# Optimization experiments

Measured on AMD Instinct MI355X. Metric: run time of the kernel, lower is better.

The kernel has to match this reference:

```python
import jax, jax.numpy as jnp
import numpy as np

B, TE, TD, H = 8, 512, 256, 256  # batch, enc len, dec len, hidden (He==Hd)

def setup_inputs() -> dict:
    key = jax.random.key(0)
    k1, k2, k3, k4, k5 = jax.random.split(key, 5)
    # Keras 'uniform' initializer: U(-0.05, 0.05)
    u = lambda k, s: jax.random.uniform(k, s, jnp.float32, -0.05, 0.05)
    return {
        "encoder_out_seq": jax.random.normal(k1, (B, TE, H), jnp.float32),
        "decoder_out_seq": jax.random.normal(k2, (B, TD, H), jnp.float32),
        "W_a": u(k3, (H, H)),
        "U_a": u(k4, (H, H)),
        "V_a": u(k5, (H, 1)),
    }

def reference(encoder_out_seq, decoder_out_seq, W_a, U_a, V_a):
    # Bahdanau additive attention, fully batched (same math as the per-step K.rnn loop)
    We = jnp.einsum('bih,hk->bik', encoder_out_seq, W_a)   # [B,Te,H]
    Uh = jnp.einsum('bjh,hk->bjk', decoder_out_seq, U_a)   # [B,Td,H]
    # energies: V_a^T tanh(We_i + Uh_j)  -> [B,Td,Te]
    t = jnp.tanh(We[:, None, :, :] + Uh[:, :, None, :])    # [B,Td,Te,H]
    e = jnp.einsum('bjih,h->bji', t, V_a[:, 0])             # [B,Td,Te]
    e = jax.nn.softmax(e, axis=-1)                          # softmax over encoder positions
    c = jnp.einsum('bji,bih->bjh', e, encoder_out_seq)      # [B,Td,H]
    return (c, e)
```

## Files before the change

kernel.cpp:

```cpp
#include <hip/hip_runtime.h>


#define BB 8
#define TE 512
#define TD 256
#define HH 256

#define EXP2F(x) __builtin_amdgcn_exp2f(x)
#define RCPF(x)  __builtin_amdgcn_rcpf(x)
#define KSCALE   2.8853900817779268f
#define NSC      (-2.8853900817779268f)

typedef __attribute__((ext_vector_type(8))) short short8_t;
typedef __attribute__((ext_vector_type(4))) float f32x4;

__device__ __forceinline__ unsigned short f2bf(float x) {
    unsigned int u = __float_as_uint(x);
    return (unsigned short)((u + 0x7FFFu + ((u >> 16) & 1u)) >> 16);
}
__device__ __forceinline__ float bf2f(unsigned short h) {
    return __uint_as_float(((unsigned int)h) << 16);
}

__global__ __launch_bounds__(256) void k_pre(
    const float* __restrict__ enc, const float* __restrict__ dec,
    const float* __restrict__ Wa,  const float* __restrict__ Ua,
    float* __restrict__ W4, float* __restrict__ Uhe)
{
    const int t  = threadIdx.x;
    const int it = blockIdx.x >> 2;
    const int ht = blockIdx.x & 3;
    const int i0 = it * 64;
    const int h0 = ht * 64;
    const bool is_enc = (i0 < BB * TE);
    const float* X  = is_enc ? (enc + (size_t)i0 * HH)
                             : (dec + (size_t)(i0 - BB * TE) * HH);
    const float* Wg = is_enc ? Wa : Ua;

    __shared__ unsigned short At_h[64][40], At_l[64][40];
    __shared__ unsigned short Xs_h[64][40], Xs_l[64][40];
    __shared__ float T[32][66];

    const int sr = t >> 2;
    const int sq = (t & 3) * 8;
    const int kr = t >> 3;
    const int hc = (t & 7) * 8;

    const int wv = t >> 6, l = t & 63;
    const int wh = (wv & 1) * 32;
    const int wi = (wv >> 1) * 32;
    const int fr = l & 15;
    const int fk = (l >> 4) * 8;
    const int rq = l >> 4;

    f32x4 acc[2][2];
    #pragma unroll
    for (int a0 = 0; a0 < 2; a0++)
        #pragma unroll
        for (int a1 = 0; a1 < 2; a1++)
            acc[a0][a1] = (f32x4){0.f, 0.f, 0.f, 0.f};

    float4 x0  = *(const float4*)(X + (size_t)sr * HH + sq);
    float4 x1  = *(const float4*)(X + (size_t)sr * HH + sq + 4);
    float4 wf0 = *(const float4*)(Wg + (size_t)kr * HH + h0 + hc);
    float4 wf1 = *(const float4*)(Wg + (size_t)kr * HH + h0 + hc + 4);

    #pragma unroll
    for (int c = 0; c < 8; c++) {
        short8_t xh, xl;
        {
            unsigned short h;
            h = f2bf(x0.x); xh[0] = (short)h; xl[0] = (short)f2bf(x0.x - bf2f(h));
            h = f2bf(x0.y); xh[1] = (short)h; xl[1] = (short)f2bf(x0.y - bf2f(h));
            h = f2bf(x0.z); xh[2] = (short)h; xl[2] = (short)f2bf(x0.z - bf2f(h));
            h = f2bf(x0.w); xh[3] = (short)h; xl[3] = (short)f2bf(x0.w - bf2f(h));
            h = f2bf(x1.x); xh[4] = (short)h; xl[4] = (short)f2bf(x1.x - bf2f(h));
            h = f2bf(x1.y); xh[5] = (short)h; xl[5] = (short)f2bf(x1.y - bf2f(h));
            h = f2bf(x1.z); xh[6] = (short)h; xl[6] = (short)f2bf(x1.z - bf2f(h));
            h = f2bf(x1.w); xh[7] = (short)h; xl[7] = (short)f2bf(x1.w - bf2f(h));
        }
        __syncthreads();
        *(short8_t*)&Xs_h[sr][sq] = xh;
        *(short8_t*)&Xs_l[sr][sq] = xl;
        {
            float2 a, b;
            a.x = wf0.x; a.y = wf0.y; b.x = wf0.z; b.y = wf0.w;
            *(float2*)&T[kr][hc]     = a;
            *(float2*)&T[kr][hc + 2] = b;
            a.x = wf1.x; a.y = wf1.y; b.x = wf1.z; b.y = wf1.w;
            *(float2*)&T[kr][hc + 4] = a;
            *(float2*)&T[kr][hc + 6] = b;
        }
        __syncthreads();
        {
            short8_t ah_, al_;
            #pragma unroll
            for (int e = 0; e < 8; e++) {
                float f = T[sq + e][sr];
                unsigned short h = f2bf(f);
                ah_[e] = (short)h;
                al_[e] = (short)f2bf(f - bf2f(h));
            }
            *(short8_t*)&At_h[sr][sq] = ah_;
            *(short8_t*)&At_l[sr][sq] = al_;
        }
        if (c < 7) {
            const int kc = (c + 1) * 32;
            x0  = *(const float4*)(X + (size_t)sr * HH + kc + sq);
            x1  = *(const float4*)(X + (size_t)sr * HH + kc + sq + 4);
            wf0 = *(const float4*)(Wg + (size_t)(kc + kr) * HH + h0 + hc);
            wf1 = *(const float4*)(Wg + (size_t)(kc + kr) * HH + h0 + hc + 4);
        }
        __syncthreads();
        #pragma unroll
        for (int fm = 0; fm < 2; fm++) {
            short8_t a_h = *(const short8_t*)&At_h[wh + 16 * fm + fr][fk];
            short8_t a_l = *(const short8_t*)&At_l[wh + 16 * fm + fr][fk];
            #pragma unroll
            for (int fn = 0; fn < 2; fn++) {
                short8_t b_h = *(const short8_t*)&Xs_h[wi + 16 * fn + fr][fk];
                short8_t b_l = *(const short8_t*)&Xs_l[wi + 16 * fn + fr][fk];
                acc[fm][fn] = __builtin_amdgcn_mfma_f32_16x16x32_bf16(a_h, b_h, acc[fm][fn], 0, 0, 0);
                acc[fm][fn] = __builtin_amdgcn_mfma_f32_16x16x32_bf16(a_h, b_l, acc[fm][fn], 0, 0, 0);
                acc[fm][fn] = __builtin_amdgcn_mfma_f32_16x16x32_bf16(a_l, b_h, acc[fm][fn], 0, 0, 0);
            }
        }
    }

    #pragma unroll
    for (int fm = 0; fm < 2; fm++) {
        #pragma unroll
        for (int fn = 0; fn < 2; fn++) {
            f32x4 v = acc[fm][fn];
            float4 o;
            o.x = EXP2F(v[0] * KSCALE);
            o.y = EXP2F(v[1] * KSCALE);
            o.z = EXP2F(v[2] * KSCALE);
            o.w = EXP2F(v[3] * KSCALE);
            const int ig = i0 + wi + 16 * fn + fr;
            const int hb = h0 + wh + 16 * fm + rq * 4;
            if (is_enc) {
                const int b  = ig >> 9;
                const int ib = ig & 511;
                const int hq = hb >> 2;
                *(float4*)(W4 + (((size_t)b * 64 + hq) * TE + ib) * 4) = o;
            } else {
                const int j = ig - BB * TE;
                *(float4*)(Uhe + (size_t)j * HH + hb) = o;
            }
        }
    }
}

__global__ __launch_bounds__(512) void k_attn(
    const float* __restrict__ enc, const float* __restrict__ W4,
    const float* __restrict__ Uhe, const float* __restrict__ Va,
    float* __restrict__ out_c, float* __restrict__ out_e)
{
    const int wv = threadIdx.x >> 6, lane = threadIdx.x & 63;
    const int b   = blockIdx.x & 7;
    const int j0  = (blockIdx.x >> 3) * 4;
    const int jj0 = b * TD + j0;

    __shared__ float sP[4][TE];
    __shared__ float sR[8][4][HH];

    const int i = (wv << 6) + lane;
    const float* wp = W4 + ((size_t)b * 64 * TE + i) * 4;
    const float* ua = Uhe + (size_t)jj0 * HH;
    const float* va = Va;

    float a0 = 0.f, a1 = 0.f, a2 = 0.f, a3 = 0.f;

#define QSTEP(ACC, U)                                                     \
    {                                                                     \
        float A_ = fmaf(w4.x, (U).x, 1.f);                                \
        float B_ = fmaf(w4.y, (U).y, 1.f);                                \
        float C_ = fmaf(w4.z, (U).z, 1.f);                                \
        float D_ = fmaf(w4.w, (U).w, 1.f);                                \
        float dAB = A_ * B_, dCD = C_ * D_;                               \
        float nAB = fmaf(v4.x, B_, v4.y * A_);                            \
        float nCD = fmaf(v4.z, D_, v4.w * C_);                            \
        float num = fmaf(nAB, dCD, nCD * dAB);                            \
        ACC = fmaf(num, RCPF(dAB * dCD), ACC);                            \
    }

#define ASTEP(Q, W4V)                                                     \
    {                                                                     \
        float4 w4 = W4V;                                                  \
        float4 v4 = *(const float4*)(va + 4 * (Q));                       \
        float4 u0 = *(const float4*)(ua + 4 * (Q));                       \
        float4 u1 = *(const float4*)(ua + HH + 4 * (Q));                  \
        float4 u2 = *(const float4*)(ua + 2 * HH + 4 * (Q));              \
        float4 u3 = *(const float4*)(ua + 3 * HH + 4 * (Q));              \
        QSTEP(a0, u0)                                                     \
        QSTEP(a1, u1)                                                     \
        QSTEP(a2, u2)                                                     \
        QSTEP(a3, u3)                                                     \
    }

    float4 wA = *(const float4*)(wp);
    float4 wB = *(const float4*)(wp + (size_t)TE * 4);
    for (int q = 0; q < 64; q += 2) {
        float4 wC = *(const float4*)(wp + (size_t)(q + 2) * TE * 4);
        float4 wD = *(const float4*)(wp + (size_t)(q + 3) * TE * 4);
        ASTEP(q, wA)
        ASTEP(q + 1, wB)
        wA = wC; wB = wD;
    }
#undef ASTEP
#undef QSTEP

    sP[0][i] = NSC * a0;
    sP[1][i] = NSC * a1;
    sP[2][i] = NSC * a2;
    sP[3][i] = NSC * a3;
    __syncthreads();

    if (wv < 4) {
        float ev[8];
        float m = -3.0e38f;
        #pragma unroll
        for (int k = 0; k < 8; k++) {
            ev[k] = sP[wv][lane + 64 * k];
            m = fmaxf(m, ev[k]);
        }
        #pragma unroll
        for (int off = 32; off; off >>= 1) m = fmaxf(m, __shfl_xor(m, off, 64));
        float s = 0.f;
        #pragma unroll
        for (int k = 0; k < 8; k++) { ev[k] = EXP2F(ev[k] - m); s += ev[k]; }
        #pragma unroll
        for (int off = 32; off; off >>= 1) s += __shfl_xor(s, off, 64);
        float rs = RCPF(s);
        float* oe = out_e + (size_t)(jj0 + wv) * TE;
        #pragma unroll
        for (int k = 0; k < 8; k++) {
            float p = ev[k] * rs;
            sP[wv][lane + 64 * k] = p;
            oe[lane + 64 * k] = p;
        }
    }
    __syncthreads();

    const int ib = wv << 6;
    const float* eb = enc + ((size_t)b * TE + ib) * HH + 4 * lane;
    float4 c0 = {0,0,0,0}, c1 = {0,0,0,0}, c2 = {0,0,0,0}, c3 = {0,0,0,0};

#define BSTEP(K, QV)                                                      \
    {                                                                     \
        float p0 = sP[0][ib + (K)];                                       \
        float p1 = sP[1][ib + (K)];                                       \
        float p2 = sP[2][ib + (K)];                                       \
        float p3 = sP[3][ib + (K)];                                       \
        float4 q = QV;                                                    \
        c0.x = fmaf(p0, q.x, c0.x); c0.y = fmaf(p0, q.y, c0.y);           \
        c0.z = fmaf(p0, q.z, c0.z); c0.w = fmaf(p0, q.w, c0.w);           \
        c1.x = fmaf(p1, q.x, c1.x); c1.y = fmaf(p1, q.y, c1.y);           \
        c1.z = fmaf(p1, q.z, c1.z); c1.w = fmaf(p1, q.w, c1.w);           \
        c2.x = fmaf(p2, q.x, c2.x); c2.y = fmaf(p2, q.y, c2.y);           \
        c2.z = fmaf(p2, q.z, c2.z); c2.w = fmaf(p2, q.w, c2.w);           \
        c3.x = fmaf(p3, q.x, c3.x); c3.y = fmaf(p3, q.y, c3.y);           \
        c3.z = fmaf(p3, q.z, c3.z); c3.w = fmaf(p3, q.w, c3.w);           \
    }

    float4 qA = *(const float4*)(eb);
    float4 qB = *(const float4*)(eb + (size_t)HH);
    for (int k = 0; k < 64; k += 2) {
        const int k2 = (k + 2 < 64) ? k + 2 : 62;
        const int k3 = (k + 3 < 64) ? k + 3 : 63;
        float4 qC = *(const float4*)(eb + (size_t)k2 * HH);
        float4 qD = *(const float4*)(eb + (size_t)k3 * HH);
        BSTEP(k, qA)
        BSTEP(k + 1, qB)
        qA = qC; qB = qD;
    }
#undef BSTEP

    *(float4*)&sR[wv][0][4 * lane] = c0;
    *(float4*)&sR[wv][1][4 * lane] = c1;
    *(float4*)&sR[wv][2][4 * lane] = c2;
    *(float4*)&sR[wv][3][4 * lane] = c3;
    __syncthreads();

    {
        const int jr = wv & 3;
        const int h2 = (wv >> 2) * 128 + 2 * lane;
        float sx = 0.f, sy = 0.f;
        #pragma unroll
        for (int ww = 0; ww < 8; ww++) {
            float2 tv = *(const float2*)&sR[ww][jr][h2];
            sx += tv.x; sy += tv.y;
        }
        float2 o; o.x = sx; o.y = sy;
        *(float2*)(out_c + (size_t)(jj0 + jr) * HH + h2) = o;
    }
}

extern "C" void kernel_launch(void* const* d_in, const int* in_sizes, int n_in,
                              void* d_out, int out_size, void* d_ws, size_t ws_size,
                              hipStream_t stream) {
    const float* enc = (const float*)d_in[0];
    const float* dec = (const float*)d_in[1];
    const float* Wa  = (const float*)d_in[2];
    const float* Ua  = (const float*)d_in[3];
    const float* Va  = (const float*)d_in[4];

    float* W4  = (float*)d_ws;
    float* Uhe = W4 + (size_t)BB * HH * TE;

    float* out_c = (float*)d_out;
    float* out_e = out_c + (size_t)BB * TD * HH;

    k_pre<<<384, 256, 0, stream>>>(enc, dec, Wa, Ua, W4, Uhe);
    k_attn<<<BB * TD / 4, 512, 0, stream>>>(enc, W4, Uhe, Va, out_c, out_e);
}
```

Baseline: 107.8 us.

## Interleave exp tables into 8-wide groups and use packed FP32 math in energy loop

The precompute kernel now writes exp(We) and exp(Uh) in an interleaved 8-float layout that pairs two H-lanes, matching the pairing of the two MFMA fragments. The attention kernel then evaluates the tanh-sum rational form with two-wide float vectors so the compiler can emit packed FMA/mul instructions, halving the scalar VALU op count. V_a is permuted into shared memory to match the new order. This adds a shared-memory staging step and a barrier, and the reciprocals remain scalar.

```diff
diff --git a/kernel.cpp b/kernel.cpp
--- a/kernel.cpp
+++ b/kernel.cpp
@@ -13,6 +13,8 @@
 
 typedef __attribute__((ext_vector_type(8))) short short8_t;
 typedef __attribute__((ext_vector_type(4))) float f32x4;
+typedef __attribute__((ext_vector_type(2))) float f32x2;
+#define PKFMA(a, b, c) __builtin_elementwise_fma((a), (b), (c))
 
 __device__ __forceinline__ unsigned short f2bf(float x) {
     unsigned int u = __float_as_uint(x);
@@ -25,7 +27,7 @@
 __global__ __launch_bounds__(256) void k_pre(
     const float* __restrict__ enc, const float* __restrict__ dec,
     const float* __restrict__ Wa,  const float* __restrict__ Ua,
-    float* __restrict__ W4, float* __restrict__ Uhe)
+    float* __restrict__ W8, float* __restrict__ Uhe2)
 {
     const int t  = threadIdx.x;
     const int it = blockIdx.x >> 2;
@@ -127,34 +129,38 @@
         }
     }
 
+    const int Q0 = (h0 + wh + rq * 4) >> 2;
+    const int p  = ((Q0 >> 3) << 2) | (Q0 & 3);
     #pragma unroll
-    for (int fm = 0; fm < 2; fm++) {
-        #pragma unroll
-        for (int fn = 0; fn < 2; fn++) {
-            f32x4 v = acc[fm][fn];
-            float4 o;
-            o.x = EXP2F(v[0] * KSCALE);
-            o.y = EXP2F(v[1] * KSCALE);
-            o.z = EXP2F(v[2] * KSCALE);
-            o.w = EXP2F(v[3] * KSCALE);
-            const int ig = i0 + wi + 16 * fn + fr;
-            const int hb = h0 + wh + 16 * fm + rq * 4;
-            if (is_enc) {
-                const int b  = ig >> 9;
-                const int ib = ig & 511;
-                const int hq = hb >> 2;
-                *(float4*)(W4 + (((size_t)b * 64 + hq) * TE + ib) * 4) = o;
-            } else {
-                const int j = ig - BB * TE;
-                *(float4*)(Uhe + (size_t)j * HH + hb) = o;
-            }
+    for (int fn = 0; fn < 2; fn++) {
+        f32x4 v0 = acc[0][fn], v1 = acc[1][fn];
+        float4 e0, e1;
+        e0.x = EXP2F(v0[0] * KSCALE); e0.y = EXP2F(v0[1] * KSCALE);
+        e0.z = EXP2F(v0[2] * KSCALE); e0.w = EXP2F(v0[3] * KSCALE);
+        e1.x = EXP2F(v1[0] * KSCALE); e1.y = EXP2F(v1[1] * KSCALE);
+        e1.z = EXP2F(v1[2] * KSCALE); e1.w = EXP2F(v1[3] * KSCALE);
+        float4 lo, hi;
+        lo.x = e0.x; lo.y = e1.x; lo.z = e0.y; lo.w = e1.y;
+        hi.x = e0.z; hi.y = e1.z; hi.z = e0.w; hi.w = e1.w;
+        const int ig = i0 + wi + 16 * fn + fr;
+        if (is_enc) {
+            const int b  = ig >> 9;
+            const int ib = ig & 511;
+            float* dst = W8 + (((size_t)b * 32 + p) * TE + ib) * 8;
+            *(float4*)dst       = lo;
+            *(float4*)(dst + 4) = hi;
+        } else {
+            const int j = ig - BB * TE;
+            float* dst = Uhe2 + (size_t)j * HH + p * 8;
+            *(float4*)dst       = lo;
+            *(float4*)(dst + 4) = hi;
         }
     }
 }
 
 __global__ __launch_bounds__(512) void k_attn(
-    const float* __restrict__ enc, const float* __restrict__ W4,
-    const float* __restrict__ Uhe, const float* __restrict__ Va,
+    const float* __restrict__ enc, const float* __restrict__ W8,
+    const float* __restrict__ Uhe2, const float* __restrict__ Va,
     float* __restrict__ out_c, float* __restrict__ out_e)
 {
     const int wv = threadIdx.x >> 6, lane = threadIdx.x & 63;
@@ -164,57 +170,62 @@
 
     __shared__ float sP[4][TE];
     __shared__ float sR[8][4][HH];
+    __shared__ float sVi[32][8];
+
+    if (threadIdx.x < 256) {
+        const int p = threadIdx.x >> 3, r = threadIdx.x & 7;
+        sVi[p][r] = Va[32 * (p >> 2) + 4 * (p & 3) + 16 * (r & 1) + (r >> 1)];
+    }
+    __syncthreads();
 
     const int i = (wv << 6) + lane;
-    const float* wp = W4 + ((size_t)b * 64 * TE + i) * 4;
-    const float* ua = Uhe + (size_t)jj0 * HH;
-    const float* va = Va;
-
-    float a0 = 0.f, a1 = 0.f, a2 = 0.f, a3 = 0.f;
-
-#define QSTEP(ACC, U)                                                     \
-    {                                                                     \
-        float A_ = fmaf(w4.x, (U).x, 1.f);                                \
-        float B_ = fmaf(w4.y, (U).y, 1.f);                                \
-        float C_ = fmaf(w4.z, (U).z, 1.f);                                \
-        float D_ = fmaf(w4.w, (U).w, 1.f);                                \
-        float dAB = A_ * B_, dCD = C_ * D_;                               \
-        float nAB = fmaf(v4.x, B_, v4.y * A_);                            \
-        float nCD = fmaf(v4.z, D_, v4.w * C_);                            \
-        float num = fmaf(nAB, dCD, nCD * dAB);                            \
-        ACC = fmaf(num, RCPF(dAB * dCD), ACC);                            \
-    }
-
-#define ASTEP(Q, W4V)                                                     \
-    {                                                                     \
-        float4 w4 = W4V;                                                  \
-        float4 v4 = *(const float4*)(va + 4 * (Q));                       \
-        float4 u0 = *(const float4*)(ua + 4 * (Q));                       \
-        float4 u1 = *(const float4*)(ua + HH + 4 * (Q));                  \
-        float4 u2 = *(const float4*)(ua + 2 * HH + 4 * (Q));              \
-        float4 u3 = *(const float4*)(ua + 3 * HH + 4 * (Q));              \
-        QSTEP(a0, u0)                                                     \
-        QSTEP(a1, u1)                                                     \
-        QSTEP(a2, u2)                                                     \
-        QSTEP(a3, u3)                                                     \
-    }
-
-    float4 wA = *(const float4*)(wp);
-    float4 wB = *(const float4*)(wp + (size_t)TE * 4);
-    for (int q = 0; q < 64; q += 2) {
-        float4 wC = *(const float4*)(wp + (size_t)(q + 2) * TE * 4);
-        float4 wD = *(const float4*)(wp + (size_t)(q + 3) * TE * 4);
-        ASTEP(q, wA)
-        ASTEP(q + 1, wB)
-        wA = wC; wB = wD;
-    }
-#undef ASTEP
-#undef QSTEP
-
-    sP[0][i] = NSC * a0;
-    sP[1][i] = NSC * a1;
-    sP[2][i] = NSC * a2;
-    sP[3][i] = NSC * a3;
+    const float* wp = W8 + ((size_t)b * 32 * TE + i) * 8;
+    const float* ua = Uhe2 + (size_t)jj0 * HH;
+
+    f32x2 acc[4];
+    #pragma unroll
+    for (int j = 0; j < 4; j++) acc[j] = (f32x2){0.f, 0.f};
+    const f32x2 one = (f32x2){1.f, 1.f};
+
+    float4 wl  = *(const float4*)(wp);
+    float4 wh_ = *(const float4*)(wp + 4);
+    for (int p = 0; p < 32; p++) {
+        const int pn = (p < 31) ? p + 1 : 31;
+        float4 nl = *(const float4*)(wp + (size_t)pn * TE * 8);
+        float4 nh = *(const float4*)(wp + (size_t)pn * TE * 8 + 4);
+        float4 vlo = *(const float4*)&sVi[p][0];
+        float4 vhi = *(const float4*)&sVi[p][4];
+        f32x2 wx = {wl.x, wl.y},   wy = {wl.z, wl.w};
+        f32x2 wz = {wh_.x, wh_.y}, ww = {wh_.z, wh_.w};
+        f32x2 vx = {vlo.x, vlo.y}, vy = {vlo.z, vlo.w};
+        f32x2 vz = {vhi.x, vhi.y}, vw = {vhi.z, vhi.w};
+        #pragma unroll
+        for (int j = 0; j < 4; j++) {
+            float4 ulo = *(const float4*)(ua + j * HH + p * 8);
+            float4 uhi = *(const float4*)(ua + j * HH + p * 8 + 4);
+            f32x2 ux = {ulo.x, ulo.y}, uy = {ulo.z, ulo.w};
+            f32x2 uz = {uhi.x, uhi.y}, uw = {uhi.z, uhi.w};
+            f32x2 A_ = PKFMA(wx, ux, one);
+            f32x2 B_ = PKFMA(wy, uy, one);
+            f32x2 C_ = PKFMA(wz, uz, one);
+            f32x2 D_ = PKFMA(ww, uw, one);
+            f32x2 dAB = A_ * B_, dCD = C_ * D_;
+            f32x2 nAB = PKFMA(vx, B_, vy * A_);
+            f32x2 nCD = PKFMA(vz, D_, vw * C_);
+            f32x2 num = PKFMA(nAB, dCD, nCD * dAB);
+            f32x2 den = dAB * dCD;
+            f32x2 r;
+            r.x = RCPF(den.x);
+            r.y = RCPF(den.y);
+            acc[j] = PKFMA(num, r, acc[j]);
+        }
+        wl = nl; wh_ = nh;
+    }
+
+    sP[0][i] = NSC * (acc[0].x + acc[0].y);
+    sP[1][i] = NSC * (acc[1].x + acc[1].y);
+    sP[2][i] = NSC * (acc[2].x + acc[2].y);
+    sP[3][i] = NSC * (acc[3].x + acc[3].y);
     __syncthreads();
 
     if (wv < 4) {
@@ -306,12 +317,12 @@
     const float* Ua  = (const float*)d_in[3];
     const float* Va  = (const float*)d_in[4];
 
-    float* W4  = (float*)d_ws;
-    float* Uhe = W4 + (size_t)BB * HH * TE;
+    float* W8   = (float*)d_ws;
+    float* Uhe2 = W8 + (size_t)BB * HH * TE;
 
     float* out_c = (float*)d_out;
     float* out_e = out_c + (size_t)BB * TD * HH;
 
-    k_pre<<<384, 256, 0, stream>>>(enc, dec, Wa, Ua, W4, Uhe);
-    k_attn<<<BB * TD / 4, 512, 0, stream>>>(enc, W4, Uhe, Va, out_c, out_e);
-}
+    k_pre<<<384, 256, 0, stream>>>(enc, dec, Wa, Ua, W8, Uhe2);
+    k_attn<<<BB * TD / 4, 512, 0, stream>>>(enc, W8, Uhe2, Va, out_c, out_e);
+}
```

Result: no change. 107.2 us (-0.6%).

## Store encoder projection row-major and split hidden dim across lanes with shuffle reduction

Applied to the files above, without the earlier changes.

The pre-kernel now writes both projections row-major into one buffer instead of a transposed h-quad-major layout for the encoder part. The attention kernel splits the hidden dimension across 16 lanes, so each lane holds its decoder-projection and V slices in registers, and reduces partial energies with xor shuffles. This removes the per-iteration reloads of U and V in the inner loop and makes the encoder-projection reads contiguous. The cost is extra shuffle reductions, a select, and partially idle lanes when writing scores to shared memory.

```diff
diff --git a/kernel.cpp b/kernel.cpp
--- a/kernel.cpp
+++ b/kernel.cpp
@@ -25,7 +25,7 @@
 __global__ __launch_bounds__(256) void k_pre(
     const float* __restrict__ enc, const float* __restrict__ dec,
     const float* __restrict__ Wa,  const float* __restrict__ Ua,
-    float* __restrict__ W4, float* __restrict__ Uhe)
+    float* __restrict__ Wout)
 {
     const int t  = threadIdx.x;
     const int it = blockIdx.x >> 2;
@@ -139,21 +139,13 @@
             o.w = EXP2F(v[3] * KSCALE);
             const int ig = i0 + wi + 16 * fn + fr;
             const int hb = h0 + wh + 16 * fm + rq * 4;
-            if (is_enc) {
-                const int b  = ig >> 9;
-                const int ib = ig & 511;
-                const int hq = hb >> 2;
-                *(float4*)(W4 + (((size_t)b * 64 + hq) * TE + ib) * 4) = o;
-            } else {
-                const int j = ig - BB * TE;
-                *(float4*)(Uhe + (size_t)j * HH + hb) = o;
-            }
+            *(float4*)(Wout + (size_t)ig * HH + hb) = o;
         }
     }
 }
 
 __global__ __launch_bounds__(512) void k_attn(
-    const float* __restrict__ enc, const float* __restrict__ W4,
+    const float* __restrict__ enc, const float* __restrict__ W4r,
     const float* __restrict__ Uhe, const float* __restrict__ Va,
     float* __restrict__ out_c, float* __restrict__ out_e)
 {
@@ -161,60 +153,77 @@
     const int b   = blockIdx.x & 7;
     const int j0  = (blockIdx.x >> 3) * 4;
     const int jj0 = b * TD + j0;
+    const int ig  = lane >> 4;
+    const int hg  = lane & 15;
 
     __shared__ float sP[4][TE];
     __shared__ float sR[8][4][HH];
 
-    const int i = (wv << 6) + lane;
-    const float* wp = W4 + ((size_t)b * 64 * TE + i) * 4;
-    const float* ua = Uhe + (size_t)jj0 * HH;
-    const float* va = Va;
-
-    float a0 = 0.f, a1 = 0.f, a2 = 0.f, a3 = 0.f;
-
-#define QSTEP(ACC, U)                                                     \
+    const float* ua = Uhe + (size_t)jj0 * HH + hg * 4;
+    const float* va = Va + hg * 4;
+    float4 v0 = *(const float4*)(va);
+    float4 v1 = *(const float4*)(va + 64);
+    float4 v2 = *(const float4*)(va + 128);
+    float4 v3 = *(const float4*)(va + 192);
+    float4 u00 = *(const float4*)(ua);
+    float4 u01 = *(const float4*)(ua + 64);
+    float4 u02 = *(const float4*)(ua + 128);
+    float4 u03 = *(const float4*)(ua + 192);
+    float4 u10 = *(const float4*)(ua + HH);
+    float4 u11 = *(const float4*)(ua + HH + 64);
+    float4 u12 = *(const float4*)(ua + HH + 128);
+    float4 u13 = *(const float4*)(ua + HH + 192);
+    float4 u20 = *(const float4*)(ua + 2 * HH);
+    float4 u21 = *(const float4*)(ua + 2 * HH + 64);
+    float4 u22 = *(const float4*)(ua + 2 * HH + 128);
+    float4 u23 = *(const float4*)(ua + 2 * HH + 192);
+    float4 u30 = *(const float4*)(ua + 3 * HH);
+    float4 u31 = *(const float4*)(ua + 3 * HH + 64);
+    float4 u32 = *(const float4*)(ua + 3 * HH + 128);
+    float4 u33 = *(const float4*)(ua + 3 * HH + 192);
+
+    const float* wp = W4r + ((size_t)(b * TE) + (wv << 6) + ig) * HH + hg * 4;
+
+#define QSTEP(ACC, WQ, VQ, UQ)                                            \
     {                                                                     \
-        float A_ = fmaf(w4.x, (U).x, 1.f);                                \
-        float B_ = fmaf(w4.y, (U).y, 1.f);                                \
-        float C_ = fmaf(w4.z, (U).z, 1.f);                                \
-        float D_ = fmaf(w4.w, (U).w, 1.f);                                \
+        float A_ = fmaf((WQ).x, (UQ).x, 1.f);                             \
+        float B_ = fmaf((WQ).y, (UQ).y, 1.f);                             \
+        float C_ = fmaf((WQ).z, (UQ).z, 1.f);                             \
+        float D_ = fmaf((WQ).w, (UQ).w, 1.f);                             \
         float dAB = A_ * B_, dCD = C_ * D_;                               \
-        float nAB = fmaf(v4.x, B_, v4.y * A_);                            \
-        float nCD = fmaf(v4.z, D_, v4.w * C_);                            \
+        float nAB = fmaf((VQ).x, B_, (VQ).y * A_);                        \
+        float nCD = fmaf((VQ).z, D_, (VQ).w * C_);                        \
         float num = fmaf(nAB, dCD, nCD * dAB);                            \
         ACC = fmaf(num, RCPF(dAB * dCD), ACC);                            \
     }
 
-#define ASTEP(Q, W4V)                                                     \
-    {                                                                     \
-        float4 w4 = W4V;                                                  \
-        float4 v4 = *(const float4*)(va + 4 * (Q));                       \
-        float4 u0 = *(const float4*)(ua + 4 * (Q));                       \
-        float4 u1 = *(const float4*)(ua + HH + 4 * (Q));                  \
-        float4 u2 = *(const float4*)(ua + 2 * HH + 4 * (Q));              \
-        float4 u3 = *(const float4*)(ua + 3 * HH + 4 * (Q));              \
-        QSTEP(a0, u0)                                                     \
-        QSTEP(a1, u1)                                                     \
-        QSTEP(a2, u2)                                                     \
-        QSTEP(a3, u3)                                                     \
-    }
-
-    float4 wA = *(const float4*)(wp);
-    float4 wB = *(const float4*)(wp + (size_t)TE * 4);
-    for (int q = 0; q < 64; q += 2) {
-        float4 wC = *(const float4*)(wp + (size_t)(q + 2) * TE * 4);
-        float4 wD = *(const float4*)(wp + (size_t)(q + 3) * TE * 4);
-        ASTEP(q, wA)
-        ASTEP(q + 1, wB)
-        wA = wC; wB = wD;
-    }
-#undef ASTEP
+    #pragma unroll 2
+    for (int it = 0; it < 16; it++) {
+        const float* wrow = wp + (size_t)(it << 2) * HH;
+        float4 w0 = *(const float4*)(wrow);
+        float4 w1 = *(const float4*)(wrow + 64);
+        float4 w2 = *(const float4*)(wrow + 128);
+        float4 w3 = *(const float4*)(wrow + 192);
+        float a0 = 0.f, a1 = 0.f, a2 = 0.f, a3 = 0.f;
+        QSTEP(a0, w0, v0, u00) QSTEP(a0, w1, v1, u01)
+        QSTEP(a0, w2, v2, u02) QSTEP(a0, w3, v3, u03)
+        QSTEP(a1, w0, v0, u10) QSTEP(a1, w1, v1, u11)
+        QSTEP(a1, w2, v2, u12) QSTEP(a1, w3, v3, u13)
+        QSTEP(a2, w0, v0, u20) QSTEP(a2, w1, v1, u21)
+        QSTEP(a2, w2, v2, u22) QSTEP(a2, w3, v3, u23)
+        QSTEP(a3, w0, v0, u30) QSTEP(a3, w1, v1, u31)
+        QSTEP(a3, w2, v2, u32) QSTEP(a3, w3, v3, u33)
+        #pragma unroll
+        for (int off = 1; off <= 8; off <<= 1) {
+            a0 += __shfl_xor(a0, off, 64);
+            a1 += __shfl_xor(a1, off, 64);
+            a2 += __shfl_xor(a2, off, 64);
+            a3 += __shfl_xor(a3, off, 64);
+        }
+        float outv = hg == 0 ? a0 : (hg == 1 ? a1 : (hg == 2 ? a2 : a3));
+        if (hg < 4) sP[hg][(wv << 6) + (it << 2) + ig] = NSC * outv;
+    }
 #undef QSTEP
-
-    sP[0][i] = NSC * a0;
-    sP[1][i] = NSC * a1;
-    sP[2][i] = NSC * a2;
-    sP[3][i] = NSC * a3;
     __syncthreads();
 
     if (wv < 4) {
@@ -306,12 +315,13 @@
     const float* Ua  = (const float*)d_in[3];
     const float* Va  = (const float*)d_in[4];
 
-    float* W4  = (float*)d_ws;
-    float* Uhe = W4 + (size_t)BB * HH * TE;
+    float* Wout = (float*)d_ws;
+    float* W4r  = Wout;
+    float* Uhe  = Wout + (size_t)BB * TE * HH;
 
     float* out_c = (float*)d_out;
     float* out_e = out_c + (size_t)BB * TD * HH;
 
-    k_pre<<<384, 256, 0, stream>>>(enc, dec, Wa, Ua, W4, Uhe);
-    k_attn<<<BB * TD / 4, 512, 0, stream>>>(enc, W4, Uhe, Va, out_c, out_e);
-}
+    k_pre<<<384, 256, 0, stream>>>(enc, dec, Wa, Ua, Wout);
+    k_attn<<<BB * TD / 4, 512, 0, stream>>>(enc, W4r, Uhe, Va, out_c, out_e);
+}
```

Result: slower. 118.0 us (+9.5%).
